# Kernel optimization log

Measured on AMD Instinct MI355X. Metric: run time of the kernel, lower is better.

The kernel has to match this reference:

```python
import jax, jax.numpy as jnp
import numpy as np

N_NODES = 100000
N_EDGES = 1600000


def gcn_conv(x, W, b, src, dst, n_nodes):
    # PyG GCNConv: h = X W; out_i = sum_j norm_ij * h_j + b, with
    # norm_ij = deg_i^{-1/2} deg_j^{-1/2} over A + I (self-loops already appended).
    h = x @ W                                   # [N, F_out]
    deg = jax.ops.segment_sum(jnp.ones(src.shape[0], x.dtype), dst,
                              num_segments=n_nodes)          # [N]
    dinv = jax.lax.rsqrt(jnp.maximum(deg, 1.0))              # deg >= 1 (self-loops)
    norm = dinv[src] * dinv[dst]                             # [E]
    msg = h[src] * norm[:, None]                             # gather + scale
    out = jax.ops.segment_sum(msg, dst, num_segments=n_nodes)
    return out + b


def setup_inputs() -> dict:
    key = jax.random.key(0)
    k1, k2, k3, k4 = jax.random.split(key, 4)
    x = jax.random.normal(k1, (N_NODES, 500), dtype=jnp.float32)
    edge_index = jax.random.randint(k2, (2, N_EDGES), 0, N_NODES, dtype=jnp.int64)
    W1 = jax.random.normal(k3, (500, 64), dtype=jnp.float32) * (1.0 / np.sqrt(500))
    b1 = jnp.zeros((64,), dtype=jnp.float32)
    W2 = jax.random.normal(k4, (64, 40), dtype=jnp.float32) * (1.0 / np.sqrt(64))
    b2 = jnp.zeros((40,), dtype=jnp.float32)
    return {"x": x, "edge_index": edge_index, "W1": W1, "b1": b1, "W2": W2, "b2": b2}


def reference(x, edge_index, W1, b1, W2, b2):
    n = x.shape[0]
    loops = jnp.arange(n, dtype=edge_index.dtype)
    src = jnp.concatenate([edge_index[0], loops])
    dst = jnp.concatenate([edge_index[1], loops])
    h = jax.nn.relu(gcn_conv(x, W1, b1, src, dst, n))
    # dropout is identity in eval mode (training=False)
    h = gcn_conv(h, W2, b2, src, dst, n)
    return jax.nn.log_softmax(h, axis=1)
```

## Files before the change

### kernel.cpp

```cpp
#include <hip/hip_runtime.h>
#include <hip/hip_bf16.h>
#include <math.h>

#define NNODES 100000
#define F_IN   500
#define F_MID  64
#define F_OUT  40
#define KPAD   512
#define H2S    48

#define BSH    7
#define NBUCK  782
#define EPB    8192
#define K4CACHE 3072

typedef __attribute__((ext_vector_type(8))) short short8;
typedef __attribute__((ext_vector_type(4))) float f32x4;

__device__ __forceinline__ unsigned short f2bf(float f) {
    union { float f; unsigned u; } c; c.f = f;
    unsigned r = c.u + 0x7FFF + ((c.u >> 16) & 1);
    return (unsigned short)(r >> 16);
}
__device__ __forceinline__ float bf2f(unsigned short u) {
    union { unsigned v; float f; } c; c.v = ((unsigned)u) << 16; return c.f;
}


__global__ __launch_bounds__(256) void bucket_count(const int* __restrict__ dst,
                                                    int* __restrict__ bcnt, int E) {
    __shared__ int h[NBUCK];
    int tid = threadIdx.x;
    for (int b = tid; b < NBUCK; b += 256) h[b] = 0;
    __syncthreads();
    int base = blockIdx.x * EPB;
#pragma unroll
    for (int j = 0; j < EPB / 256; j++) {
        int e = base + j * 256 + tid;
        if (e < E) atomicAdd(&h[dst[e] >> BSH], 1);
    }
    __syncthreads();
    for (int b = tid; b < NBUCK; b += 256) {
        int c = h[b];
        if (c) atomicAdd(&bcnt[b], c);
    }
}

__global__ __launch_bounds__(1024) void bucket_scan(const int* __restrict__ bcnt,
                                                    int* __restrict__ bstart,
                                                    int* __restrict__ bcur, int E) {
    __shared__ int wsum[16];
    int t = threadIdx.x, lane = t & 63, w = t >> 6;
    int v = (t < NBUCK) ? bcnt[t] : 0;
    int s = v;
#pragma unroll
    for (int off = 1; off < 64; off <<= 1) {
        int u = __shfl_up(s, off, 64);
        if (lane >= off) s += u;
    }
    if (lane == 63) wsum[w] = s;
    __syncthreads();
    if (w == 0) {
        int ws = (lane < 16) ? wsum[lane] : 0;
#pragma unroll
        for (int off = 1; off < 16; off <<= 1) {
            int u = __shfl_up(ws, off, 64);
            if (lane >= off) ws += u;
        }
        if (lane < 16) wsum[lane] = ws;
    }
    __syncthreads();
    int excl = s - v + ((w > 0) ? wsum[w - 1] : 0);
    if (t < NBUCK) { bstart[t] = excl; bcur[t] = excl; }
    if (t == 0) bstart[NBUCK] = E;
}

__global__ __launch_bounds__(256) void bucket_scatter(const int* __restrict__ src,
                                                      const int* __restrict__ dst,
                                                      int* __restrict__ bcur,
                                                      int* __restrict__ stage, int E) {
    __shared__ int h[NBUCK];
    __shared__ int lcur[NBUCK];
    int tid = threadIdx.x;
    for (int b = tid; b < NBUCK; b += 256) h[b] = 0;
    __syncthreads();
    int base = blockIdx.x * EPB;
#pragma unroll
    for (int j = 0; j < EPB / 256; j++) {
        int e = base + j * 256 + tid;
        if (e < E) atomicAdd(&h[dst[e] >> BSH], 1);
    }
    __syncthreads();
    int rot = (blockIdx.x * 97) % NBUCK;
    for (int i = tid; i < NBUCK; i += 256) {
        int b = i + rot; if (b >= NBUCK) b -= NBUCK;
        int c = h[b];
        lcur[b] = c ? atomicAdd(&bcur[b], c) : 0;
    }
    __syncthreads();
#pragma unroll
    for (int j = 0; j < EPB / 256; j++) {
        int e = base + j * 256 + tid;
        if (e < E) {
            int d = dst[e];
            int pos = atomicAdd(&lcur[d >> BSH], 1);
            stage[pos] = ((d & 127) << 17) | src[e];
        }
    }
}

__global__ __launch_bounds__(256) void bucket_fill(const int* __restrict__ stage,
                                                   const int* __restrict__ bstart,
                                                   int* __restrict__ row_start,
                                                   float* __restrict__ dinv,
                                                   int* __restrict__ csr_src, int E) {
    __shared__ int cnt[128];
    __shared__ int wtot[2];
    __shared__ int cache[K4CACHE];
    int tid = threadIdx.x;
    int b = blockIdx.x;
    int s0 = bstart[b], s1 = bstart[b + 1];
    int nE = s1 - s0;
    if (tid < 128) cnt[tid] = 0;
    __syncthreads();
    bool cached = (nE <= K4CACHE);
    for (int i = tid; i < nE; i += 256) {
        int v = stage[s0 + i];
        if (cached) cache[i] = v;
        atomicAdd(&cnt[v >> 17], 1);
    }
    __syncthreads();
    int n = (b << BSH) + tid;
    bool valid = (tid < 128) && (n < NNODES);
    int c = (tid < 128) ? cnt[tid] : 0;
    int add = valid ? (c + 1) : 0;
    int s = add;
    int lane = tid & 63;
#pragma unroll
    for (int off = 1; off < 64; off <<= 1) {
        int u = __shfl_up(s, off, 64);
        if (lane >= off) s += u;
    }
    if (tid < 128 && lane == 63) wtot[tid >> 6] = s;
    __syncthreads();
    int excl = s - add + ((tid >= 64 && tid < 128) ? wtot[0] : 0);
    int basep = s0 + (b << BSH) + excl;
    if (valid) {
        row_start[n] = basep;
        dinv[n] = rsqrtf((float)(c + 1));
        csr_src[basep] = n;
        cnt[tid] = basep + 1;
    }
    if (b == NBUCK - 1 && tid == 0) row_start[NNODES] = E + NNODES;
    __syncthreads();
    for (int i = tid; i < nE; i += 256) {
        int v = cached ? cache[i] : stage[s0 + i];
        int pos = atomicAdd(&cnt[v >> 17], 1);
        csr_src[pos] = v & 0x1FFFF;
    }
}

__global__ void w1t_prep(const float* __restrict__ W1, unsigned short* __restrict__ W1T) {
    int idx = blockIdx.x * blockDim.x + threadIdx.x;
    if (idx >= F_MID * KPAD) return;
    int n = idx >> 9;
    int k = idx & (KPAD - 1);
    float v = (k < F_IN) ? W1[k * F_MID + n] : 0.f;
    W1T[idx] = f2bf(v);
}

__global__ void w2t_prep(const float* __restrict__ W2, unsigned short* __restrict__ W2T) {
    int idx = blockIdx.x * blockDim.x + threadIdx.x;
    if (idx >= H2S * F_MID) return;
    int c = idx >> 6;
    int k = idx & 63;
    float v = (c < F_OUT) ? W2[k * F_OUT + c] : 0.f;
    W2T[idx] = f2bf(v);
}

__global__ __launch_bounds__(256) void gemm1_kernel(const float* __restrict__ X,
                                                    const unsigned short* __restrict__ W1T,
                                                    const float* __restrict__ dinv,
                                                    unsigned short* __restrict__ h1b) {
    const int BM = 128, BK = 32;
    __shared__ __align__(16) unsigned short A_lds[BM][BK];
    __shared__ __align__(16) unsigned short B_lds[F_MID][BK];

    int tid  = threadIdx.x;
    int wave = tid >> 6;
    int lane = tid & 63;
    int block_row = blockIdx.x * BM;

    int ar = tid >> 1, ah = tid & 1;
    int agr = block_row + ar;
    if (agr >= NNODES) agr = NNODES - 1;
    const float* xrow = X + (size_t)agr * F_IN;
    int bn = tid >> 2, bc = tid & 3;

    int mcol = lane & 15, quad = lane >> 4;

    f32x4 acc[2][4];
#pragma unroll
    for (int t = 0; t < 2; t++)
#pragma unroll
        for (int c = 0; c < 4; c++) {
            f32x4 z = {0.f, 0.f, 0.f, 0.f};
            acc[t][c] = z;
        }

    float4 apf[4];
    uint4  bpf;
    auto load_tile = [&](int ks) {
#pragma unroll
        for (int i = 0; i < 4; i++) {
            int kg = ks * BK + ah * 16 + i * 4;
            if (kg < F_IN) apf[i] = *(const float4*)(xrow + kg);
            else           apf[i] = make_float4(0.f, 0.f, 0.f, 0.f);
        }
        bpf = *(const uint4*)(W1T + (size_t)bn * KPAD + ks * BK + bc * 8);
    };

    load_tile(0);

    const int NK = KPAD / BK;
    for (int ks = 0; ks < NK; ks++) {
        unsigned pk[8];
#pragma unroll
        for (int i = 0; i < 4; i++) {
            pk[2 * i]     = (unsigned)f2bf(apf[i].x) | ((unsigned)f2bf(apf[i].y) << 16);
            pk[2 * i + 1] = (unsigned)f2bf(apf[i].z) | ((unsigned)f2bf(apf[i].w) << 16);
        }
        *(uint4*)&A_lds[ar][ah * 16]     = make_uint4(pk[0], pk[1], pk[2], pk[3]);
        *(uint4*)&A_lds[ar][ah * 16 + 8] = make_uint4(pk[4], pk[5], pk[6], pk[7]);
        *(uint4*)&B_lds[bn][bc * 8] = bpf;
        __syncthreads();

        if (ks + 1 < NK) load_tile(ks + 1);

        short8 a0 = *(const short8*)&A_lds[wave * 32 + mcol][quad * 8];
        short8 a1 = *(const short8*)&A_lds[wave * 32 + 16 + mcol][quad * 8];
        short8 bf[4];
#pragma unroll
        for (int c = 0; c < 4; c++)
            bf[c] = *(const short8*)&B_lds[c * 16 + mcol][quad * 8];

#pragma unroll
        for (int c = 0; c < 4; c++) {
            acc[0][c] = __builtin_amdgcn_mfma_f32_16x16x32_bf16(a0, bf[c], acc[0][c], 0, 0, 0);
            acc[1][c] = __builtin_amdgcn_mfma_f32_16x16x32_bf16(a1, bf[c], acc[1][c], 0, 0, 0);
        }
        __syncthreads();
    }

#pragma unroll
    for (int t = 0; t < 2; t++)
#pragma unroll
        for (int reg = 0; reg < 4; reg++) {
            int gr = block_row + wave * 32 + t * 16 + quad * 4 + reg;
            if (gr < NNODES) {
                float sc = dinv[gr];
#pragma unroll
                for (int c = 0; c < 4; c++)
                    h1b[(size_t)gr * F_MID + c * 16 + mcol] = f2bf(acc[t][c][reg] * sc);
            }
        }
}

__global__ __launch_bounds__(256) void agg1_kernel(const unsigned short* __restrict__ h1b,
                                                   const int* __restrict__ csr_src,
                                                   const int* __restrict__ row_start,
                                                   const float* __restrict__ dinv,
                                                   const float* __restrict__ b1,
                                                   unsigned short* __restrict__ out1b) {
    int tid = threadIdx.x;
    int node = blockIdx.x * 4 + (tid >> 6);
    int lane = tid & 63;

    int s0 = row_start[node], s1 = row_start[node + 1];
    float acc = 0.f;

    int idx[8];
    int e = s0;
#pragma unroll
    for (int j = 0; j < 8; j++) {
        int p = e + j; if (p > s1 - 1) p = s1 - 1;
        idx[j] = csr_src[p];
    }
    while (e < s1) {
        int cnt = s1 - e;
        int cidx[8];
#pragma unroll
        for (int j = 0; j < 8; j++) cidx[j] = idx[j];
        int en = e + 8;
        if (en < s1) {
#pragma unroll
            for (int j = 0; j < 8; j++) {
                int p = en + j; if (p > s1 - 1) p = s1 - 1;
                idx[j] = csr_src[p];
            }
        }
#pragma unroll
        for (int j = 0; j < 8; j++) {
            float v = bf2f(h1b[(size_t)cidx[j] * F_MID + lane]);
            if (j < cnt) acc += v;
        }
        e = en;
    }

    float dn = dinv[node];
    float v = fmaxf(acc * dn + b1[lane], 0.f);
    out1b[(size_t)node * F_MID + lane] = f2bf(v);
}

__global__ __launch_bounds__(256) void gemm2_kernel(const unsigned short* __restrict__ out1b,
                                                    const unsigned short* __restrict__ W2T,
                                                    const float* __restrict__ dinv,
                                                    unsigned short* __restrict__ h2b) {
    int tid = threadIdx.x;
    int wave = tid >> 6;
    int lane = tid & 63;
    int n0 = blockIdx.x * 64 + wave * 16;
    int m = lane & 15, quad = lane >> 4;

    int arow = n0 + m; if (arow >= NNODES) arow = NNODES - 1;

    f32x4 acc[3];
#pragma unroll
    for (int c = 0; c < 3; c++) { f32x4 z = {0.f, 0.f, 0.f, 0.f}; acc[c] = z; }

#pragma unroll
    for (int t = 0; t < 2; t++) {
        short8 a = *(const short8*)&out1b[(size_t)arow * F_MID + t * 32 + quad * 8];
#pragma unroll
        for (int c = 0; c < 3; c++) {
            short8 b = *(const short8*)&W2T[(size_t)(c * 16 + m) * F_MID + t * 32 + quad * 8];
            acc[c] = __builtin_amdgcn_mfma_f32_16x16x32_bf16(a, b, acc[c], 0, 0, 0);
        }
    }

#pragma unroll
    for (int reg = 0; reg < 4; reg++) {
        int gr = n0 + quad * 4 + reg;
        if (gr < NNODES) {
            float dn = dinv[gr];
#pragma unroll
            for (int c = 0; c < 3; c++)
                h2b[(size_t)gr * H2S + c * 16 + m] = f2bf(acc[c][reg] * dn);
        }
    }
}

__global__ __launch_bounds__(256) void agg2_softmax_kernel(const unsigned short* __restrict__ h2b,
                                                           const int* __restrict__ csr_src,
                                                           const int* __restrict__ row_start,
                                                           const float* __restrict__ dinv,
                                                           const float* __restrict__ b2,
                                                           float* __restrict__ out) {
    int tid = threadIdx.x;
    int node = blockIdx.x * 4 + (tid >> 6);
    int lane = tid & 63;
    int cl = (lane < H2S) ? lane : 0;

    int s0 = row_start[node], s1 = row_start[node + 1];
    float acc = 0.f;

    int idx[8];
    int e = s0;
#pragma unroll
    for (int j = 0; j < 8; j++) {
        int p = e + j; if (p > s1 - 1) p = s1 - 1;
        idx[j] = csr_src[p];
    }
    while (e < s1) {
        int cnt = s1 - e;
        int cidx[8];
#pragma unroll
        for (int j = 0; j < 8; j++) cidx[j] = idx[j];
        int en = e + 8;
        if (en < s1) {
#pragma unroll
            for (int j = 0; j < 8; j++) {
                int p = en + j; if (p > s1 - 1) p = s1 - 1;
                idx[j] = csr_src[p];
            }
        }
#pragma unroll
        for (int j = 0; j < 8; j++) {
            float v = bf2f(h2b[(size_t)cidx[j] * H2S + cl]);
            if (j < cnt) acc += v;
        }
        e = en;
    }

    float dn = dinv[node];
    bool act = (lane < F_OUT);
    float z = act ? (acc * dn + b2[cl]) : -3.4e38f;
    float m = z;
#pragma unroll
    for (int off = 1; off < 64; off <<= 1) m = fmaxf(m, __shfl_xor(m, off, 64));
    float p = act ? __expf(z - m) : 0.f;
#pragma unroll
    for (int off = 1; off < 64; off <<= 1) p += __shfl_xor(p, off, 64);
    float lse = m + logf(p);
    if (act) out[(size_t)node * F_OUT + lane] = z - lse;
}

extern "C" void kernel_launch(void* const* d_in, const int* in_sizes, int n_in,
                              void* d_out, int out_size, void* d_ws, size_t ws_size,
                              hipStream_t stream) {
    const float* X   = (const float*)d_in[0];
    const int*   ei  = (const int*)d_in[1];
    const float* W1  = (const float*)d_in[2];
    const float* b1  = (const float*)d_in[3];
    const float* W2  = (const float*)d_in[4];
    const float* b2  = (const float*)d_in[5];
    float* out = (float*)d_out;

    const int N = NNODES;
    const int E = in_sizes[1] / 2;
    const int TOTAL = E + N;
    const int* srcv = ei;
    const int* dstv = ei + E;

    char* p = (char*)d_ws;
    auto carve = [&](size_t bytes) {
        void* r = (void*)p;
        p += (bytes + 255) & ~(size_t)255;
        return r;
    };
    int*   bcnt      = (int*)carve((size_t)NBUCK * 4);
    int*   bstart    = (int*)carve((size_t)(NBUCK + 1) * 4);
    int*   bcur      = (int*)carve((size_t)NBUCK * 4);
    int*   stage     = (int*)carve((size_t)E * 4);
    int*   row_start = (int*)carve((size_t)(N + 1) * 4);
    int*   csr_src   = (int*)carve((size_t)TOTAL * 4);
    float* dinv      = (float*)carve((size_t)N * 4);
    unsigned short* W1T  = (unsigned short*)carve((size_t)F_MID * KPAD * 2);
    unsigned short* W2T  = (unsigned short*)carve((size_t)H2S * F_MID * 2);
    unsigned short* h1b  = (unsigned short*)carve((size_t)N * F_MID * 2);
    unsigned short* out1b= (unsigned short*)carve((size_t)N * F_MID * 2);
    unsigned short* h2b  = (unsigned short*)carve((size_t)N * H2S * 2);
    (void)ws_size; (void)n_in; (void)out_size;

    const int GB = (E + EPB - 1) / EPB;

    hipMemsetAsync(bcnt, 0, (size_t)NBUCK * 4, stream);
    bucket_count<<<GB, 256, 0, stream>>>(dstv, bcnt, E);
    bucket_scan<<<1, 1024, 0, stream>>>(bcnt, bstart, bcur, E);
    bucket_scatter<<<GB, 256, 0, stream>>>(srcv, dstv, bcur, stage, E);
    bucket_fill<<<NBUCK, 256, 0, stream>>>(stage, bstart, row_start, dinv, csr_src, E);

    w1t_prep<<<(F_MID * KPAD + 255) / 256, 256, 0, stream>>>(W1, W1T);
    w2t_prep<<<(H2S * F_MID + 255) / 256, 256, 0, stream>>>(W2, W2T);

    gemm1_kernel<<<(N + 127) / 128, 256, 0, stream>>>(X, W1T, dinv, h1b);
    agg1_kernel<<<N / 4, 256, 0, stream>>>(h1b, csr_src, row_start, dinv, b1, out1b);
    gemm2_kernel<<<(N + 63) / 64, 256, 0, stream>>>(out1b, W2T, dinv, h2b);
    agg2_softmax_kernel<<<N / 4, 256, 0, stream>>>(h2b, csr_src, row_start, dinv, b2, out);
}
```

Measured before the change: 524.1 us.

## Rewrite gemm1 to load MFMA fragments directly from global, dropping LDS

The first GEMM no longer stages X and W1T tiles through shared memory with block-wide barriers. Each wave now loads its A fragment directly from X in registers, converts it to bf16, and reads W1T fragments straight from global memory, where the small weight matrix should stay cache-resident. The block tile shrinks from 128 to 64 rows, with launch bounds requesting more resident blocks. This removes barrier and LDS traffic but gives up the explicit prefetch double-buffering and relies on the cache for the repeated W1T reads.

```diff
diff --git a/kernel.cpp b/kernel.cpp
--- a/kernel.cpp
+++ b/kernel.cpp
@@ -178,92 +178,61 @@
     W2T[idx] = f2bf(v);
 }
 
-__global__ __launch_bounds__(256) void gemm1_kernel(const float* __restrict__ X,
-                                                    const unsigned short* __restrict__ W1T,
-                                                    const float* __restrict__ dinv,
-                                                    unsigned short* __restrict__ h1b) {
-    const int BM = 128, BK = 32;
-    __shared__ __align__(16) unsigned short A_lds[BM][BK];
-    __shared__ __align__(16) unsigned short B_lds[F_MID][BK];
-
-    int tid  = threadIdx.x;
+__global__ __launch_bounds__(256, 4) void gemm1_kernel(const float* __restrict__ X,
+                                                       const unsigned short* __restrict__ W1T,
+                                                       const float* __restrict__ dinv,
+                                                       unsigned short* __restrict__ h1b) {
+    int tid = threadIdx.x;
     int wave = tid >> 6;
     int lane = tid & 63;
-    int block_row = blockIdx.x * BM;
-
-    int ar = tid >> 1, ah = tid & 1;
-    int agr = block_row + ar;
-    if (agr >= NNODES) agr = NNODES - 1;
-    const float* xrow = X + (size_t)agr * F_IN;
-    int bn = tid >> 2, bc = tid & 3;
-
-    int mcol = lane & 15, quad = lane >> 4;
-
-    f32x4 acc[2][4];
-#pragma unroll
-    for (int t = 0; t < 2; t++)
+    int m = lane & 15, quad = lane >> 4;
+    int n0 = blockIdx.x * 64 + wave * 16;
+
+    int arow = n0 + m; if (arow >= NNODES) arow = NNODES - 1;
+    const float* xrow = X + (size_t)arow * F_IN;
+
+    f32x4 acc[4];
+#pragma unroll
+    for (int c = 0; c < 4; c++) { f32x4 z = {0.f, 0.f, 0.f, 0.f}; acc[c] = z; }
+
+    const int NK = KPAD / 32;
+#pragma unroll 4
+    for (int ks = 0; ks < NK; ks++) {
+        int kg = ks * 32 + quad * 8;
+        float4 a0, a1;
+        if (kg < F_IN)     a0 = *(const float4*)(xrow + kg);
+        else               a0 = make_float4(0.f, 0.f, 0.f, 0.f);
+        if (kg + 4 < F_IN) a1 = *(const float4*)(xrow + kg + 4);
+        else               a1 = make_float4(0.f, 0.f, 0.f, 0.f);
+
+        unsigned pk[4];
+        pk[0] = (unsigned)f2bf(a0.x) | ((unsigned)f2bf(a0.y) << 16);
+        pk[1] = (unsigned)f2bf(a0.z) | ((unsigned)f2bf(a0.w) << 16);
+        pk[2] = (unsigned)f2bf(a1.x) | ((unsigned)f2bf(a1.y) << 16);
+        pk[3] = (unsigned)f2bf(a1.z) | ((unsigned)f2bf(a1.w) << 16);
+        short8 a;
+        *(unsigned*)&((short*)&a)[0] = pk[0];
+        *(unsigned*)&((short*)&a)[2] = pk[1];
+        *(unsigned*)&((short*)&a)[4] = pk[2];
+        *(unsigned*)&((short*)&a)[6] = pk[3];
+
 #pragma unroll
         for (int c = 0; c < 4; c++) {
-            f32x4 z = {0.f, 0.f, 0.f, 0.f};
-            acc[t][c] = z;
-        }
-
-    float4 apf[4];
-    uint4  bpf;
-    auto load_tile = [&](int ks) {
-#pragma unroll
-        for (int i = 0; i < 4; i++) {
-            int kg = ks * BK + ah * 16 + i * 4;
-            if (kg < F_IN) apf[i] = *(const float4*)(xrow + kg);
-            else           apf[i] = make_float4(0.f, 0.f, 0.f, 0.f);
-        }
-        bpf = *(const uint4*)(W1T + (size_t)bn * KPAD + ks * BK + bc * 8);
-    };
-
-    load_tile(0);
-
-    const int NK = KPAD / BK;
-    for (int ks = 0; ks < NK; ks++) {
-        unsigned pk[8];
-#pragma unroll
-        for (int i = 0; i < 4; i++) {
-            pk[2 * i]     = (unsigned)f2bf(apf[i].x) | ((unsigned)f2bf(apf[i].y) << 16);
-            pk[2 * i + 1] = (unsigned)f2bf(apf[i].z) | ((unsigned)f2bf(apf[i].w) << 16);
-        }
-        *(uint4*)&A_lds[ar][ah * 16]     = make_uint4(pk[0], pk[1], pk[2], pk[3]);
-        *(uint4*)&A_lds[ar][ah * 16 + 8] = make_uint4(pk[4], pk[5], pk[6], pk[7]);
-        *(uint4*)&B_lds[bn][bc * 8] = bpf;
-        __syncthreads();
-
-        if (ks + 1 < NK) load_tile(ks + 1);
-
-        short8 a0 = *(const short8*)&A_lds[wave * 32 + mcol][quad * 8];
-        short8 a1 = *(const short8*)&A_lds[wave * 32 + 16 + mcol][quad * 8];
-        short8 bf[4];
-#pragma unroll
-        for (int c = 0; c < 4; c++)
-            bf[c] = *(const short8*)&B_lds[c * 16 + mcol][quad * 8];
-
-#pragma unroll
-        for (int c = 0; c < 4; c++) {
-            acc[0][c] = __builtin_amdgcn_mfma_f32_16x16x32_bf16(a0, bf[c], acc[0][c], 0, 0, 0);
-            acc[1][c] = __builtin_amdgcn_mfma_f32_16x16x32_bf16(a1, bf[c], acc[1][c], 0, 0, 0);
-        }
-        __syncthreads();
-    }
-
-#pragma unroll
-    for (int t = 0; t < 2; t++)
-#pragma unroll
-        for (int reg = 0; reg < 4; reg++) {
-            int gr = block_row + wave * 32 + t * 16 + quad * 4 + reg;
-            if (gr < NNODES) {
-                float sc = dinv[gr];
-#pragma unroll
-                for (int c = 0; c < 4; c++)
-                    h1b[(size_t)gr * F_MID + c * 16 + mcol] = f2bf(acc[t][c][reg] * sc);
-            }
-        }
+            short8 b = *(const short8*)&W1T[(size_t)(c * 16 + m) * KPAD + ks * 32 + quad * 8];
+            acc[c] = __builtin_amdgcn_mfma_f32_16x16x32_bf16(a, b, acc[c], 0, 0, 0);
+        }
+    }
+
+#pragma unroll
+    for (int reg = 0; reg < 4; reg++) {
+        int gr = n0 + quad * 4 + reg;
+        if (gr < NNODES) {
+            float sc = dinv[gr];
+#pragma unroll
+            for (int c = 0; c < 4; c++)
+                h1b[(size_t)gr * F_MID + c * 16 + m] = f2bf(acc[c][reg] * sc);
+        }
+    }
 }
 
 __global__ __launch_bounds__(256) void agg1_kernel(const unsigned short* __restrict__ h1b,
@@ -453,7 +422,7 @@
     w1t_prep<<<(F_MID * KPAD + 255) / 256, 256, 0, stream>>>(W1, W1T);
     w2t_prep<<<(H2S * F_MID + 255) / 256, 256, 0, stream>>>(W2, W2T);
 
-    gemm1_kernel<<<(N + 127) / 128, 256, 0, stream>>>(X, W1T, dinv, h1b);
+    gemm1_kernel<<<(N + 63) / 64, 256, 0, stream>>>(X, W1T, dinv, h1b);
     agg1_kernel<<<N / 4, 256, 0, stream>>>(h1b, csr_src, row_start, dinv, b1, out1b);
     gemm2_kernel<<<(N + 63) / 64, 256, 0, stream>>>(out1b, W2T, dinv, h2b);
     agg2_softmax_kernel<<<N / 4, 256, 0, stream>>>(h2b, csr_src, row_start, dinv, b2, out);
```

New measurement: 537.0 us. 1.02x slower.
